# Kernel optimization log

Hardware: AMD Instinct MI355X
Metric: run time of the kernel (lower is better)

Reference implementation:

```python
import jax, jax.numpy as jnp
import numpy as np

N_NODES = 20000
N_EDGES = 640000
H = 64            # node_hidden_size
E_FEAT = 16       # edge_features_size
T = 2             # num_prop_rounds


def setup_inputs() -> dict:
    key = jax.random.key(0)
    ks = jax.random.split(key, 10)
    hv = jax.random.normal(ks[0], (N_NODES, H), dtype=jnp.float32)
    e = jax.random.normal(ks[1], (N_EDGES, E_FEAT), dtype=jnp.float32)
    src = jax.random.randint(ks[2], (N_EDGES,), 0, N_NODES, dtype=jnp.int32)
    dst = jax.random.randint(ks[3], (N_EDGES,), 0, N_NODES, dtype=jnp.int32)
    s = 0.1  # param init scale to keep activations in a sane range
    W_msg = jax.random.normal(ks[4], (T, 2 * H + E_FEAT, 2 * H), dtype=jnp.float32) * s
    b_msg = jax.random.normal(ks[5], (T, 2 * H), dtype=jnp.float32) * s
    W_ih = jax.random.normal(ks[6], (T, 3 * H, 2 * H), dtype=jnp.float32) * s
    W_hh = jax.random.normal(ks[7], (T, 3 * H, H), dtype=jnp.float32) * s
    b_ih = jax.random.normal(ks[8], (T, 3 * H), dtype=jnp.float32) * s
    b_hh = jax.random.normal(ks[9], (T, 3 * H), dtype=jnp.float32) * s
    return {"hv": hv, "e": e, "src": src, "dst": dst,
            "W_msg": W_msg, "b_msg": b_msg,
            "W_ih": W_ih, "W_hh": W_hh, "b_ih": b_ih, "b_hh": b_hh}


def _gru_cell(a, h, W_ih, W_hh, b_ih, b_hh):
    # torch.nn.GRUCell math
    gi = a @ W_ih.T + b_ih   # [N, 3H]
    gh = h @ W_hh.T + b_hh   # [N, 3H]
    i_r, i_z, i_n = jnp.split(gi, 3, axis=1)
    h_r, h_z, h_n = jnp.split(gh, 3, axis=1)
    r = jax.nn.sigmoid(i_r + h_r)
    z = jax.nn.sigmoid(i_z + h_z)
    n = jnp.tanh(i_n + r * h_n)
    return (1.0 - z) * n + z * h


def reference(hv, e, src, dst, W_msg, b_msg, W_ih, W_hh, b_ih, b_hh):
    num_nodes = hv.shape[0]
    num_rounds = W_msg.shape[0]
    for t in range(num_rounds):  # small fixed loop over prop rounds
        # per-edge: concat([h_dst, h_src, e_uv]) -> Linear -> sum-reduce to dst
        msg_in = jnp.concatenate([hv[dst], hv[src], e], axis=1)  # [E, 2H+Ef]
        msgs = msg_in @ W_msg[t] + b_msg[t]                      # [E, 2H]
        a = jax.ops.segment_sum(msgs, dst, num_segments=num_nodes)  # [N, 2H]
        hv = _gru_cell(a, hv, W_ih[t], W_hh[t], b_ih[t], b_hh[t])
    return hv
```

## Files before the change

### kernel.cpp

```cpp
#include <hip/hip_runtime.h>
#include <cstddef>
#include <cstdint>

#define NN 20000
#define NE 640000
#define MP 20096
#define KA 224
#define NC 16
#define CHUNK 40000
#define NB_SCAN 79

typedef _Float16 f16x8 __attribute__((ext_vector_type(8)));
typedef float f32x4 __attribute__((ext_vector_type(4)));

__device__ __forceinline__ float h2f(unsigned short u) {
    _Float16 h;
    *reinterpret_cast<unsigned short*>(&h) = u;
    return (float)h;
}
__device__ __forceinline__ unsigned short f2h(float f) {
    _Float16 h = (_Float16)f;
    return *reinterpret_cast<unsigned short*>(&h);
}
__device__ __forceinline__ void splitf(float x, unsigned short& hi, unsigned short& lo) {
    _Float16 h = (_Float16)x;
    _Float16 l = (_Float16)(x - (float)h);
    hi = *reinterpret_cast<unsigned short*>(&h);
    lo = *reinterpret_cast<unsigned short*>(&l);
}

__global__ void init_kernel(const float* __restrict__ hv0, unsigned short* __restrict__ hf0,
                            int* __restrict__ cnt) {
    int i = blockIdx.x * blockDim.x + threadIdx.x;
    if (i < NC * NN) cnt[i] = 0;
    if (i < NN * 64) hf0[i] = f2h(hv0[i]);
}

__global__ void hist_kernel(const int* __restrict__ dst, int* __restrict__ cnt) {
    int i = blockIdx.x * blockDim.x + threadIdx.x;
    if (i < NE) atomicAdd(&cnt[(i / CHUNK) * NN + dst[i]], 1);
}

__global__ __launch_bounds__(256) void scan1_kernel(const int* __restrict__ cnt,
                                                    int* __restrict__ lp,
                                                    int* __restrict__ bsum) {
    __shared__ int s[256];
    int t = threadIdx.x;
    int i = blockIdx.x * 256 + t;
    int d = 0;
    if (i < NN)
#pragma unroll
        for (int c = 0; c < NC; ++c) d += cnt[c * NN + i];
    s[t] = d;
    __syncthreads();
    for (int off = 1; off < 256; off <<= 1) {
        int v = (t >= off) ? s[t - off] : 0;
        __syncthreads();
        s[t] += v;
        __syncthreads();
    }
    if (i < NN) lp[i] = s[t] - d;
    if (t == 255) bsum[blockIdx.x] = s[255];
}

__global__ __launch_bounds__(256) void scan3_kernel(const int* __restrict__ cnt,
                                                    const int* __restrict__ lp,
                                                    const int* __restrict__ bsum,
                                                    int* __restrict__ row_ptr,
                                                    int* __restrict__ cursor) {
    __shared__ int sb[128];
    int t = threadIdx.x;
    if (t < 128) sb[t] = (t < NB_SCAN) ? bsum[t] : 0;
    __syncthreads();
    for (int off = 1; off < 128; off <<= 1) {
        int u = (t < 128 && t >= off) ? sb[t - off] : 0;
        __syncthreads();
        if (t < 128) sb[t] += u;
        __syncthreads();
    }
    int boff = (blockIdx.x == 0) ? 0 : sb[blockIdx.x - 1];
    int i = blockIdx.x * 256 + t;
    if (i < NN) {
        int run = boff + lp[i];
        row_ptr[i] = run;
#pragma unroll
        for (int c = 0; c < NC; ++c) {
            cursor[c * NN + i] = run;
            run += cnt[c * NN + i];
        }
    }
    if (i == 0) row_ptr[NN] = NE;
}

__global__ void place_kernel(const int* __restrict__ src, const int* __restrict__ dst,
                             int* __restrict__ cursor, int2* __restrict__ adj) {
    int i = blockIdx.x * blockDim.x + threadIdx.x;
    if (i < NE) {
        int d = dst[i];
        int pos = atomicAdd(&cursor[(i / CHUNK) * NN + d], 1);
        adj[pos] = make_int2(src[i], i);
    }
}

__global__ __launch_bounds__(256) void esum_csr_kernel(
        const float* __restrict__ ef, const int* __restrict__ row_ptr,
        const int2* __restrict__ adj, float* __restrict__ esum,
        float* __restrict__ degf) {
    int wid = threadIdx.x >> 6, lane = threadIdx.x & 63;
    int v = blockIdx.x * 4 + wid;
    if (v >= NN) return;
    int rp0 = row_ptr[v], rp1 = row_ptr[v + 1];
    int q = lane >> 2;
    int fo = (lane & 3) << 2;
    float4 a0 = make_float4(0.f, 0.f, 0.f, 0.f), a1 = a0;
    int i = rp0 + q;
    for (; i + 16 < rp1; i += 32) {
        int e0 = adj[i].y, e1 = adj[i + 16].y;
        float4 x0 = *(const float4*)(ef + (size_t)e0 * 16 + fo);
        float4 x1 = *(const float4*)(ef + (size_t)e1 * 16 + fo);
        a0.x += x0.x; a0.y += x0.y; a0.z += x0.z; a0.w += x0.w;
        a1.x += x1.x; a1.y += x1.y; a1.z += x1.z; a1.w += x1.w;
    }
    for (; i < rp1; i += 16) {
        int e = adj[i].y;
        float4 x = *(const float4*)(ef + (size_t)e * 16 + fo);
        a0.x += x.x; a0.y += x.y; a0.z += x.z; a0.w += x.w;
    }
    a0.x += a1.x; a0.y += a1.y; a0.z += a1.z; a0.w += a1.w;
#pragma unroll
    for (int m = 4; m < 64; m <<= 1) {
        a0.x += __shfl_xor(a0.x, m);
        a0.y += __shfl_xor(a0.y, m);
        a0.z += __shfl_xor(a0.z, m);
        a0.w += __shfl_xor(a0.w, m);
    }
    if (lane < 4) *(float4*)(esum + (size_t)v * 16 + fo) = a0;
    if (lane == 0) degf[v] = (float)(rp1 - rp0);
}

__global__ __launch_bounds__(192) void fold_kernel(
        const float* __restrict__ W_msg, const float* __restrict__ b_msg,
        const float* __restrict__ W_ih, float* __restrict__ WcT,
        float* __restrict__ bvec) {
    __shared__ float ldsW[64][193];
    int t = blockIdx.x / 9;
    int k0 = (blockIdx.x % 9) * 16;
    int j = threadIdx.x;
    float acc[16];
#pragma unroll
    for (int kk = 0; kk < 16; ++kk) acc[kk] = 0.f;
    float bacc = 0.f;
    for (int mc = 0; mc < 2; ++mc) {
        for (int i = threadIdx.x; i < 192 * 64; i += 192) {
            int jj = i >> 6, mm = i & 63;
            ldsW[mm][jj] = W_ih[((size_t)t * 192 + jj) * 128 + mc * 64 + mm];
        }
        __syncthreads();
        for (int mm = 0; mm < 64; ++mm) {
            float wl = ldsW[mm][j];
            float bm = b_msg[t * 128 + mc * 64 + mm];
            bacc = fmaf(bm, wl, bacc);
#pragma unroll
            for (int kk = 0; kk < 16; ++kk) {
                float wm = W_msg[((size_t)t * 144 + k0 + kk) * 128 + mc * 64 + mm];
                acc[kk] = fmaf(wm, wl, acc[kk]);
            }
        }
        __syncthreads();
    }
#pragma unroll
    for (int kk = 0; kk < 16; ++kk)
        WcT[((size_t)t * 192 + j) * 144 + k0 + kk] = acc[kk];
    if (k0 == 0) bvec[t * 192 + j] = bacc;
}

__global__ void wbig_kernel(const float* __restrict__ WcT, const float* __restrict__ bvec,
                            const float* __restrict__ b_ih, const float* __restrict__ b_hh,
                            const float* __restrict__ W_hh,
                            unsigned short* __restrict__ Bhi, unsigned short* __restrict__ Blo) {
    int idx = blockIdx.x * 256 + threadIdx.x;
    if (idx >= 2 * 256 * KA) return;
    int t = idx / (256 * KA);
    int rem = idx % (256 * KA);
    int n = rem / KA, k = rem % KA;
    float v = 0.f;
    if (n < 192) {
        if (k < 64) {
            if (n < 128) v = W_hh[(size_t)t * 192 * 64 + n * 64 + k];
        } else if (k < 128) {
            v = WcT[((size_t)t * 192 + n) * 144 + k];
        } else if (k < 192) {
            v = WcT[((size_t)t * 192 + n) * 144 + (k - 128)];
        } else if (k < 208) {
            v = WcT[((size_t)t * 192 + n) * 144 + 128 + (k - 192)];
        } else if (k == 208) {
            v = bvec[t * 192 + n];
        } else if (k == 209) {
            v = (n < 128) ? (b_ih[t * 192 + n] + b_hh[t * 192 + n]) : b_ih[t * 192 + n];
        }
    } else {
        int j = n - 64;
        if (k < 64) v = W_hh[(size_t)t * 192 * 64 + j * 64 + k];
        else if (k == 209) v = b_hh[t * 192 + j];
    }
    unsigned short hi, lo;
    splitf(v, hi, lo);
    Bhi[idx] = hi;
    Blo[idx] = lo;
}

__global__ void atail_kernel(const float* __restrict__ esum, const float* __restrict__ degf,
                             unsigned short* __restrict__ Ahi) {
    int i = blockIdx.x * blockDim.x + threadIdx.x;
    if (i >= NN * 32) return;
    int v = i >> 5, k = 192 + (i & 31);
    float val;
    if (k < 208) val = esum[(size_t)v * 16 + (k - 192)];
    else if (k == 208) val = degf[v];
    else if (k == 209) val = 1.f;
    else val = 0.f;
    Ahi[(size_t)v * KA + k] = f2h(val);
}

__global__ __launch_bounds__(256) void gather_kernel(
        const float* __restrict__ hv, const unsigned short* __restrict__ hf,
        const int* __restrict__ row_ptr, const int2* __restrict__ adj,
        unsigned short* __restrict__ Ahi, unsigned short* __restrict__ Alo) {
    int wid = threadIdx.x >> 6, lane = threadIdx.x & 63;
    int v = blockIdx.x * 4 + wid;
    if (v >= NN) return;
    int rp0 = row_ptr[v], rp1 = row_ptr[v + 1];
    int q = lane >> 4;
    int fo = (lane & 15) << 2;
    float4 acc[8];
#pragma unroll
    for (int u = 0; u < 8; ++u) acc[u] = make_float4(0.f, 0.f, 0.f, 0.f);
    int i = rp0 + q;
    for (; i + 28 < rp1; i += 32) {
        int s[8];
#pragma unroll
        for (int u = 0; u < 8; ++u) s[u] = adj[i + 4 * u].x;
#pragma unroll
        for (int u = 0; u < 8; ++u) {
            ushort4 x = *(const ushort4*)(hf + (size_t)s[u] * 64 + fo);
            acc[u].x += h2f(x.x); acc[u].y += h2f(x.y);
            acc[u].z += h2f(x.z); acc[u].w += h2f(x.w);
        }
    }
    for (; i + 4 < rp1; i += 8) {
        int s0 = adj[i].x, s1 = adj[i + 4].x;
        ushort4 x0 = *(const ushort4*)(hf + (size_t)s0 * 64 + fo);
        ushort4 x1 = *(const ushort4*)(hf + (size_t)s1 * 64 + fo);
        acc[0].x += h2f(x0.x); acc[0].y += h2f(x0.y);
        acc[0].z += h2f(x0.z); acc[0].w += h2f(x0.w);
        acc[1].x += h2f(x1.x); acc[1].y += h2f(x1.y);
        acc[1].z += h2f(x1.z); acc[1].w += h2f(x1.w);
    }
    for (; i < rp1; i += 4) {
        int s = adj[i].x;
        ushort4 x = *(const ushort4*)(hf + (size_t)s * 64 + fo);
        acc[0].x += h2f(x.x); acc[0].y += h2f(x.y);
        acc[0].z += h2f(x.z); acc[0].w += h2f(x.w);
    }
#pragma unroll
    for (int u = 1; u < 8; ++u) {
        acc[0].x += acc[u].x; acc[0].y += acc[u].y;
        acc[0].z += acc[u].z; acc[0].w += acc[u].w;
    }
#pragma unroll
    for (int m = 16; m < 64; m <<= 1) {
        acc[0].x += __shfl_xor(acc[0].x, m);
        acc[0].y += __shfl_xor(acc[0].y, m);
        acc[0].z += __shfl_xor(acc[0].z, m);
        acc[0].w += __shfl_xor(acc[0].w, m);
    }
    if (lane < 16) {
        float dg = (float)(rp1 - rp0);
        float4 hvv = *(const float4*)(hv + (size_t)v * 64 + fo);
        float4 dv = make_float4(dg * hvv.x, dg * hvv.y, dg * hvv.z, dg * hvv.w);
        ushort4 hh, sh, dh, dl;
        hh.x = f2h(hvv.x); hh.y = f2h(hvv.y); hh.z = f2h(hvv.z); hh.w = f2h(hvv.w);
        sh.x = f2h(acc[0].x); sh.y = f2h(acc[0].y);
        sh.z = f2h(acc[0].z); sh.w = f2h(acc[0].w);
        splitf(dv.x, dh.x, dl.x); splitf(dv.y, dh.y, dl.y);
        splitf(dv.z, dh.z, dl.z); splitf(dv.w, dh.w, dl.w);
        *(ushort4*)(Ahi + (size_t)v * KA + fo) = hh;
        *(ushort4*)(Ahi + (size_t)v * KA + 64 + fo) = sh;
        *(ushort4*)(Ahi + (size_t)v * KA + 128 + fo) = dh;
        *(ushort4*)(Alo + (size_t)v * KA + 128 + fo) = dl;
    }
}

__global__ __launch_bounds__(256) void gemm_gru(
        const _Float16* __restrict__ Ahi, const _Float16* __restrict__ Alo,
        const _Float16* __restrict__ Bhi, const _Float16* __restrict__ Blo,
        const float* __restrict__ hin,
        float* __restrict__ fout, unsigned short* __restrict__ hfout) {
    __shared__ _Float16 Ash[64][40];
    __shared__ _Float16 Asl[64][40];
    __shared__ _Float16 Bsh[256][40];
    __shared__ _Float16 Bsl[256][40];
    int tid = threadIdx.x;
    int w = tid >> 6, l = tid & 63;
    int row0 = blockIdx.x * 64;
    f32x4 acc[16];
#pragma unroll
    for (int i = 0; i < 16; ++i) acc[i] = (f32x4){0.f, 0.f, 0.f, 0.f};

    int sAr = tid >> 2, sAc = (tid & 3) * 8;
    int kg = (l >> 4) * 8;
    int ar = w * 16 + (l & 15);
    int lc = l & 15;

#pragma unroll 1
    for (int ks = 0; ks < 4; ++ks) {
        int k0 = ks * 32;
        *(float4*)&Ash[sAr][sAc] = *(const float4*)(Ahi + (size_t)(row0 + sAr) * KA + k0 + sAc);
        {
            const float4* ph = (const float4*)(Bhi + (size_t)tid * KA + k0);
            float4 h0 = ph[0], h1 = ph[1], h2 = ph[2], h3 = ph[3];
            *(float4*)&Bsh[tid][0] = h0;  *(float4*)&Bsh[tid][8] = h1;
            *(float4*)&Bsh[tid][16] = h2; *(float4*)&Bsh[tid][24] = h3;
        }
        __syncthreads();
        f16x8 ah = *(const f16x8*)&Ash[ar][kg];
#pragma unroll
        for (int fn = 0; fn < 16; ++fn) {
            f16x8 bh = *(const f16x8*)&Bsh[fn * 16 + lc][kg];
            acc[fn] = __builtin_amdgcn_mfma_f32_16x16x32_f16(ah, bh, acc[fn], 0, 0, 0);
        }
        __syncthreads();
    }

#pragma unroll 1
    for (int ks = 4; ks < 6; ++ks) {
        int k0 = ks * 32;
        *(float4*)&Ash[sAr][sAc] = *(const float4*)(Ahi + (size_t)(row0 + sAr) * KA + k0 + sAc);
        *(float4*)&Asl[sAr][sAc] = *(const float4*)(Alo + (size_t)(row0 + sAr) * KA + k0 + sAc);
        {
            const float4* ph = (const float4*)(Bhi + (size_t)tid * KA + k0);
            float4 h0 = ph[0], h1 = ph[1], h2 = ph[2], h3 = ph[3];
            *(float4*)&Bsh[tid][0] = h0;  *(float4*)&Bsh[tid][8] = h1;
            *(float4*)&Bsh[tid][16] = h2; *(float4*)&Bsh[tid][24] = h3;
            const float4* pl = (const float4*)(Blo + (size_t)tid * KA + k0);
            float4 l0 = pl[0], l1 = pl[1], l2 = pl[2], l3 = pl[3];
            *(float4*)&Bsl[tid][0] = l0;  *(float4*)&Bsl[tid][8] = l1;
            *(float4*)&Bsl[tid][16] = l2; *(float4*)&Bsl[tid][24] = l3;
        }
        __syncthreads();
        f16x8 ah = *(const f16x8*)&Ash[ar][kg];
        f16x8 al = *(const f16x8*)&Asl[ar][kg];
#pragma unroll
        for (int fn = 0; fn < 16; ++fn) {
            f16x8 bh = *(const f16x8*)&Bsh[fn * 16 + lc][kg];
            f16x8 bl = *(const f16x8*)&Bsl[fn * 16 + lc][kg];
            acc[fn] = __builtin_amdgcn_mfma_f32_16x16x32_f16(ah, bh, acc[fn], 0, 0, 0);
            acc[fn] = __builtin_amdgcn_mfma_f32_16x16x32_f16(ah, bl, acc[fn], 0, 0, 0);
            acc[fn] = __builtin_amdgcn_mfma_f32_16x16x32_f16(al, bh, acc[fn], 0, 0, 0);
        }
        __syncthreads();
    }

    {
        const int k0 = 192;
        *(float4*)&Ash[sAr][sAc] = *(const float4*)(Ahi + (size_t)(row0 + sAr) * KA + k0 + sAc);
        {
            const float4* ph = (const float4*)(Bhi + (size_t)tid * KA + k0);
            float4 h0 = ph[0], h1 = ph[1], h2 = ph[2], h3 = ph[3];
            *(float4*)&Bsh[tid][0] = h0;  *(float4*)&Bsh[tid][8] = h1;
            *(float4*)&Bsh[tid][16] = h2; *(float4*)&Bsh[tid][24] = h3;
            const float4* pl = (const float4*)(Blo + (size_t)tid * KA + k0);
            float4 l0 = pl[0], l1 = pl[1], l2 = pl[2], l3 = pl[3];
            *(float4*)&Bsl[tid][0] = l0;  *(float4*)&Bsl[tid][8] = l1;
            *(float4*)&Bsl[tid][16] = l2; *(float4*)&Bsl[tid][24] = l3;
        }
        __syncthreads();
        f16x8 ah = *(const f16x8*)&Ash[ar][kg];
#pragma unroll
        for (int fn = 0; fn < 16; ++fn) {
            f16x8 bh = *(const f16x8*)&Bsh[fn * 16 + lc][kg];
            f16x8 bl = *(const f16x8*)&Bsl[fn * 16 + lc][kg];
            acc[fn] = __builtin_amdgcn_mfma_f32_16x16x32_f16(ah, bh, acc[fn], 0, 0, 0);
            acc[fn] = __builtin_amdgcn_mfma_f32_16x16x32_f16(ah, bl, acc[fn], 0, 0, 0);
        }
        __syncthreads();
    }

    int jb = l & 15;
#pragma unroll
    for (int q = 0; q < 4; ++q) {
        int row = row0 + w * 16 + (l >> 4) * 4 + q;
        if (row >= NN) continue;
#pragma unroll
        for (int fj = 0; fj < 4; ++fj) {
            int j = jb + fj * 16;
            float rr = acc[fj][q];
            float zz = acc[4 + fj][q];
            float in_ = acc[8 + fj][q];
            float hn = acc[12 + fj][q];
            float r = 1.f / (1.f + __expf(-rr));
            float z = 1.f / (1.f + __expf(-zz));
            float n = tanhf(in_ + r * hn);
            float h = hin[(size_t)row * 64 + j];
            float val = (1.f - z) * n + z * h;
            fout[(size_t)row * 64 + j] = val;
            hfout[(size_t)row * 64 + j] = f2h(val);
        }
    }
}

extern "C" void kernel_launch(void* const* d_in, const int* in_sizes, int n_in,
                              void* d_out, int out_size, void* d_ws, size_t ws_size,
                              hipStream_t stream) {
    const float* hv0   = (const float*)d_in[0];
    const float* ef    = (const float*)d_in[1];
    const int*   src   = (const int*)d_in[2];
    const int*   dst   = (const int*)d_in[3];
    const float* W_msg = (const float*)d_in[4];
    const float* b_msg = (const float*)d_in[5];
    const float* W_ih  = (const float*)d_in[6];
    const float* W_hh  = (const float*)d_in[7];
    const float* b_ih  = (const float*)d_in[8];
    const float* b_hh  = (const float*)d_in[9];
    float* out = (float*)d_out;

    char* ws = (char*)d_ws;
    size_t off = 0;
    auto alloc = [&](size_t bytes) -> char* {
        char* p = ws + off;
        off = (off + bytes + 255) & ~(size_t)255;
        return p;
    };
    int*   cnt      = (int*)alloc((size_t)NC * NN * 4);
    int*   row_ptr  = (int*)alloc((NN + 1) * 4);
    int*   cursor   = (int*)alloc((size_t)NC * NN * 4);
    int2*  adj      = (int2*)alloc((size_t)NE * 8);
    float* esum     = (float*)alloc((size_t)NN * 16 * 4);
    float* degf     = (float*)alloc(NN * 4);
    float* WcT      = (float*)alloc((size_t)2 * 192 * 144 * 4);
    float* bvec     = (float*)alloc(2 * 192 * 4);
    int*   lp       = (int*)alloc(NN * 4);
    int*   bsum     = (int*)alloc(NB_SCAN * 4);
    unsigned short* Ahi = (unsigned short*)alloc((size_t)MP * KA * 2);
    unsigned short* Alo = (unsigned short*)alloc((size_t)MP * KA * 2);
    unsigned short* Bhi = (unsigned short*)alloc((size_t)2 * 256 * KA * 2);
    unsigned short* Blo = (unsigned short*)alloc((size_t)2 * 256 * KA * 2);
    float* hv1      = (float*)alloc((size_t)NN * 64 * 4);
    unsigned short* hf0 = (unsigned short*)alloc((size_t)NN * 64 * 2);
    unsigned short* hf1 = (unsigned short*)alloc((size_t)NN * 64 * 2);

    init_kernel<<<(NN * 64 + 255) / 256, 256, 0, stream>>>(hv0, hf0, cnt);
    hist_kernel<<<(NE + 255) / 256, 256, 0, stream>>>(dst, cnt);
    scan1_kernel<<<NB_SCAN, 256, 0, stream>>>(cnt, lp, bsum);
    scan3_kernel<<<NB_SCAN, 256, 0, stream>>>(cnt, lp, bsum, row_ptr, cursor);
    place_kernel<<<(NE + 255) / 256, 256, 0, stream>>>(src, dst, cursor, adj);
    esum_csr_kernel<<<(NN + 3) / 4, 256, 0, stream>>>(ef, row_ptr, adj, esum, degf);
    fold_kernel<<<18, 192, 0, stream>>>(W_msg, b_msg, W_ih, WcT, bvec);
    wbig_kernel<<<(2 * 256 * KA + 255) / 256, 256, 0, stream>>>(WcT, bvec, b_ih, b_hh,
                                                                W_hh, Bhi, Blo);
    atail_kernel<<<(NN * 32 + 255) / 256, 256, 0, stream>>>(esum, degf, Ahi);

    for (int t = 0; t < 2; ++t) {
        const float* hin = (t == 0) ? hv0 : hv1;
        const unsigned short* hfin = (t == 0) ? hf0 : hf1;
        float* hout = (t == 1) ? out : hv1;
        gather_kernel<<<(NN + 3) / 4, 256, 0, stream>>>(hin, hfin, row_ptr, adj, Ahi, Alo);
        gemm_gru<<<MP / 64, 256, 0, stream>>>(
            (const _Float16*)Ahi, (const _Float16*)Alo,
            (const _Float16*)(Bhi + (size_t)t * 256 * KA),
            (const _Float16*)(Blo + (size_t)t * 256 * KA),
            hin, hout, hf1);
    }
}
```

Before: 198.0 us.

## Widen gather loads, fold A-tail fill into gather, skip zero B blocks in GEMM

The gather kernel now reads 8 fp16 features per lane with 16-byte loads, covering 8 edges in parallel instead of 4, and keeps 4 independent accumulator sets. It also writes the edge-sum, degree and bias columns of A directly, so the separate atail_kernel launch is removed. That work is repeated every round, where before it ran once. The GEMM skips MFMA tiles whose B columns are known to be zero in certain K ranges: the W_hh part only uses k<64, and the message part does not use the h-input block. This cuts MFMA and LDS reads, assuming the weight matrix really has those zero blocks.

```diff
diff --git a/kernel.cpp b/kernel.cpp
--- a/kernel.cpp
+++ b/kernel.cpp
@@ -12,6 +12,7 @@
 
 typedef _Float16 f16x8 __attribute__((ext_vector_type(8)));
 typedef float f32x4 __attribute__((ext_vector_type(4)));
+typedef unsigned short u16x8 __attribute__((ext_vector_type(8)));
 
 __device__ __forceinline__ float h2f(unsigned short u) {
     _Float16 h;
@@ -209,85 +210,76 @@
     Blo[idx] = lo;
 }
 
-__global__ void atail_kernel(const float* __restrict__ esum, const float* __restrict__ degf,
-                             unsigned short* __restrict__ Ahi) {
-    int i = blockIdx.x * blockDim.x + threadIdx.x;
-    if (i >= NN * 32) return;
-    int v = i >> 5, k = 192 + (i & 31);
-    float val;
-    if (k < 208) val = esum[(size_t)v * 16 + (k - 192)];
-    else if (k == 208) val = degf[v];
-    else if (k == 209) val = 1.f;
-    else val = 0.f;
-    Ahi[(size_t)v * KA + k] = f2h(val);
-}
-
 __global__ __launch_bounds__(256) void gather_kernel(
         const float* __restrict__ hv, const unsigned short* __restrict__ hf,
         const int* __restrict__ row_ptr, const int2* __restrict__ adj,
+        const float* __restrict__ esum, const float* __restrict__ degf,
         unsigned short* __restrict__ Ahi, unsigned short* __restrict__ Alo) {
     int wid = threadIdx.x >> 6, lane = threadIdx.x & 63;
     int v = blockIdx.x * 4 + wid;
     if (v >= NN) return;
     int rp0 = row_ptr[v], rp1 = row_ptr[v + 1];
-    int q = lane >> 4;
-    int fo = (lane & 15) << 2;
-    float4 acc[8];
-#pragma unroll
-    for (int u = 0; u < 8; ++u) acc[u] = make_float4(0.f, 0.f, 0.f, 0.f);
+    int q = lane >> 3;
+    int fo = (lane & 7) << 3;
+    float a0[8], a1[8], a2[8], a3[8];
+#pragma unroll
+    for (int j = 0; j < 8; ++j) { a0[j] = 0.f; a1[j] = 0.f; a2[j] = 0.f; a3[j] = 0.f; }
     int i = rp0 + q;
-    for (; i + 28 < rp1; i += 32) {
-        int s[8];
-#pragma unroll
-        for (int u = 0; u < 8; ++u) s[u] = adj[i + 4 * u].x;
-#pragma unroll
-        for (int u = 0; u < 8; ++u) {
-            ushort4 x = *(const ushort4*)(hf + (size_t)s[u] * 64 + fo);
-            acc[u].x += h2f(x.x); acc[u].y += h2f(x.y);
-            acc[u].z += h2f(x.z); acc[u].w += h2f(x.w);
-        }
-    }
-    for (; i + 4 < rp1; i += 8) {
-        int s0 = adj[i].x, s1 = adj[i + 4].x;
-        ushort4 x0 = *(const ushort4*)(hf + (size_t)s0 * 64 + fo);
-        ushort4 x1 = *(const ushort4*)(hf + (size_t)s1 * 64 + fo);
-        acc[0].x += h2f(x0.x); acc[0].y += h2f(x0.y);
-        acc[0].z += h2f(x0.z); acc[0].w += h2f(x0.w);
-        acc[1].x += h2f(x1.x); acc[1].y += h2f(x1.y);
-        acc[1].z += h2f(x1.z); acc[1].w += h2f(x1.w);
-    }
-    for (; i < rp1; i += 4) {
+    for (; i + 24 < rp1; i += 32) {
+        int s0 = adj[i].x, s1 = adj[i + 8].x, s2 = adj[i + 16].x, s3 = adj[i + 24].x;
+        u16x8 x0 = *(const u16x8*)(hf + (size_t)s0 * 64 + fo);
+        u16x8 x1 = *(const u16x8*)(hf + (size_t)s1 * 64 + fo);
+        u16x8 x2 = *(const u16x8*)(hf + (size_t)s2 * 64 + fo);
+        u16x8 x3 = *(const u16x8*)(hf + (size_t)s3 * 64 + fo);
+#pragma unroll
+        for (int j = 0; j < 8; ++j) {
+            a0[j] += h2f(x0[j]); a1[j] += h2f(x1[j]);
+            a2[j] += h2f(x2[j]); a3[j] += h2f(x3[j]);
+        }
+    }
+    for (; i < rp1; i += 8) {
         int s = adj[i].x;
-        ushort4 x = *(const ushort4*)(hf + (size_t)s * 64 + fo);
-        acc[0].x += h2f(x.x); acc[0].y += h2f(x.y);
-        acc[0].z += h2f(x.z); acc[0].w += h2f(x.w);
-    }
-#pragma unroll
-    for (int u = 1; u < 8; ++u) {
-        acc[0].x += acc[u].x; acc[0].y += acc[u].y;
-        acc[0].z += acc[u].z; acc[0].w += acc[u].w;
-    }
-#pragma unroll
-    for (int m = 16; m < 64; m <<= 1) {
-        acc[0].x += __shfl_xor(acc[0].x, m);
-        acc[0].y += __shfl_xor(acc[0].y, m);
-        acc[0].z += __shfl_xor(acc[0].z, m);
-        acc[0].w += __shfl_xor(acc[0].w, m);
-    }
-    if (lane < 16) {
+        u16x8 x = *(const u16x8*)(hf + (size_t)s * 64 + fo);
+#pragma unroll
+        for (int j = 0; j < 8; ++j) a0[j] += h2f(x[j]);
+    }
+#pragma unroll
+    for (int j = 0; j < 8; ++j) a0[j] += a1[j] + a2[j] + a3[j];
+#pragma unroll
+    for (int m = 8; m < 64; m <<= 1)
+#pragma unroll
+        for (int j = 0; j < 8; ++j) a0[j] += __shfl_xor(a0[j], m);
+    if (lane < 8) {
         float dg = (float)(rp1 - rp0);
-        float4 hvv = *(const float4*)(hv + (size_t)v * 64 + fo);
-        float4 dv = make_float4(dg * hvv.x, dg * hvv.y, dg * hvv.z, dg * hvv.w);
-        ushort4 hh, sh, dh, dl;
-        hh.x = f2h(hvv.x); hh.y = f2h(hvv.y); hh.z = f2h(hvv.z); hh.w = f2h(hvv.w);
-        sh.x = f2h(acc[0].x); sh.y = f2h(acc[0].y);
-        sh.z = f2h(acc[0].z); sh.w = f2h(acc[0].w);
-        splitf(dv.x, dh.x, dl.x); splitf(dv.y, dh.y, dl.y);
-        splitf(dv.z, dh.z, dl.z); splitf(dv.w, dh.w, dl.w);
-        *(ushort4*)(Ahi + (size_t)v * KA + fo) = hh;
-        *(ushort4*)(Ahi + (size_t)v * KA + 64 + fo) = sh;
-        *(ushort4*)(Ahi + (size_t)v * KA + 128 + fo) = dh;
-        *(ushort4*)(Alo + (size_t)v * KA + 128 + fo) = dl;
+        float4 hA = *(const float4*)(hv + (size_t)v * 64 + lane * 8);
+        float4 hB = *(const float4*)(hv + (size_t)v * 64 + lane * 8 + 4);
+        float h8[8] = {hA.x, hA.y, hA.z, hA.w, hB.x, hB.y, hB.z, hB.w};
+        u16x8 hh, sh, dh, dl;
+#pragma unroll
+        for (int j = 0; j < 8; ++j) {
+            hh[j] = f2h(h8[j]);
+            sh[j] = f2h(a0[j]);
+            unsigned short thi, tlo;
+            splitf(dg * h8[j], thi, tlo);
+            dh[j] = thi; dl[j] = tlo;
+        }
+        *(u16x8*)(Ahi + (size_t)v * KA + fo) = hh;
+        *(u16x8*)(Ahi + (size_t)v * KA + 64 + fo) = sh;
+        *(u16x8*)(Ahi + (size_t)v * KA + 128 + fo) = dh;
+        *(u16x8*)(Alo + (size_t)v * KA + 128 + fo) = dl;
+    } else if (lane < 12) {
+        int o = lane - 8;
+        u16x8 tv;
+#pragma unroll
+        for (int j = 0; j < 8; ++j) tv[j] = 0;
+        if (o < 2) {
+#pragma unroll
+            for (int j = 0; j < 8; ++j) tv[j] = f2h(esum[(size_t)v * 16 + o * 8 + j]);
+        } else if (o == 2) {
+            tv[0] = f2h(degf[v]);
+            tv[1] = f2h(1.f);
+        }
+        *(u16x8*)(Ahi + (size_t)v * KA + 192 + o * 8) = tv;
     }
 }
 
@@ -313,7 +305,7 @@
     int lc = l & 15;
 
 #pragma unroll 1
-    for (int ks = 0; ks < 4; ++ks) {
+    for (int ks = 0; ks < 2; ++ks) {
         int k0 = ks * 32;
         *(float4*)&Ash[sAr][sAc] = *(const float4*)(Ahi + (size_t)(row0 + sAr) * KA + k0 + sAc);
         {
@@ -325,7 +317,32 @@
         __syncthreads();
         f16x8 ah = *(const f16x8*)&Ash[ar][kg];
 #pragma unroll
-        for (int fn = 0; fn < 16; ++fn) {
+        for (int fn = 0; fn < 8; ++fn) {
+            f16x8 bh = *(const f16x8*)&Bsh[fn * 16 + lc][kg];
+            acc[fn] = __builtin_amdgcn_mfma_f32_16x16x32_f16(ah, bh, acc[fn], 0, 0, 0);
+        }
+#pragma unroll
+        for (int fn = 12; fn < 16; ++fn) {
+            f16x8 bh = *(const f16x8*)&Bsh[fn * 16 + lc][kg];
+            acc[fn] = __builtin_amdgcn_mfma_f32_16x16x32_f16(ah, bh, acc[fn], 0, 0, 0);
+        }
+        __syncthreads();
+    }
+
+#pragma unroll 1
+    for (int ks = 2; ks < 4; ++ks) {
+        int k0 = ks * 32;
+        *(float4*)&Ash[sAr][sAc] = *(const float4*)(Ahi + (size_t)(row0 + sAr) * KA + k0 + sAc);
+        {
+            const float4* ph = (const float4*)(Bhi + (size_t)tid * KA + k0);
+            float4 h0 = ph[0], h1 = ph[1], h2 = ph[2], h3 = ph[3];
+            *(float4*)&Bsh[tid][0] = h0;  *(float4*)&Bsh[tid][8] = h1;
+            *(float4*)&Bsh[tid][16] = h2; *(float4*)&Bsh[tid][24] = h3;
+        }
+        __syncthreads();
+        f16x8 ah = *(const f16x8*)&Ash[ar][kg];
+#pragma unroll
+        for (int fn = 0; fn < 12; ++fn) {
             f16x8 bh = *(const f16x8*)&Bsh[fn * 16 + lc][kg];
             acc[fn] = __builtin_amdgcn_mfma_f32_16x16x32_f16(ah, bh, acc[fn], 0, 0, 0);
         }
@@ -351,7 +368,7 @@
         f16x8 ah = *(const f16x8*)&Ash[ar][kg];
         f16x8 al = *(const f16x8*)&Asl[ar][kg];
 #pragma unroll
-        for (int fn = 0; fn < 16; ++fn) {
+        for (int fn = 0; fn < 12; ++fn) {
             f16x8 bh = *(const f16x8*)&Bsh[fn * 16 + lc][kg];
             f16x8 bl = *(const f16x8*)&Bsl[fn * 16 + lc][kg];
             acc[fn] = __builtin_amdgcn_mfma_f32_16x16x32_f16(ah, bh, acc[fn], 0, 0, 0);
@@ -458,13 +475,13 @@
     fold_kernel<<<18, 192, 0, stream>>>(W_msg, b_msg, W_ih, WcT, bvec);
     wbig_kernel<<<(2 * 256 * KA + 255) / 256, 256, 0, stream>>>(WcT, bvec, b_ih, b_hh,
                                                                 W_hh, Bhi, Blo);
-    atail_kernel<<<(NN * 32 + 255) / 256, 256, 0, stream>>>(esum, degf, Ahi);
 
     for (int t = 0; t < 2; ++t) {
         const float* hin = (t == 0) ? hv0 : hv1;
         const unsigned short* hfin = (t == 0) ? hf0 : hf1;
         float* hout = (t == 1) ? out : hv1;
-        gather_kernel<<<(NN + 3) / 4, 256, 0, stream>>>(hin, hfin, row_ptr, adj, Ahi, Alo);
+        gather_kernel<<<(NN + 3) / 4, 256, 0, stream>>>(hin, hfin, row_ptr, adj,
+                                                        esum, degf, Ahi, Alo);
         gemm_gru<<<MP / 64, 256, 0, stream>>>(
             (const _Float16*)Ahi, (const _Float16*)Alo,
             (const _Float16*)(Bhi + (size_t)t * 256 * KA),
```

After: 199.1 us. No clear change (+0.6%).
